# Kernel tuning notes

Measured on AMD Instinct MI355X. Metric: run time of the kernel, lower is better.

Reference implementation:

```python
import jax, jax.numpy as jnp
import numpy as np

N_NODES = 100000


def _gcn_conv(x, W, b, src, dst, n):
    # PyG GCNConv: add self-loops, sym-normalize by deg^{-1/2}, then X W + b
    h = x @ W  # [N, out]
    ones = jnp.ones(src.shape[0], dtype=x.dtype)
    deg = jax.ops.segment_sum(ones, dst, num_segments=n) + 1.0  # +1 for self loop
    dinv = jax.lax.rsqrt(deg)
    norm = dinv[src] * dinv[dst]  # [E]
    agg = jax.ops.segment_sum(h[src] * norm[:, None], dst, num_segments=n)
    agg = agg + h * (dinv * dinv)[:, None]  # self-loop contribution
    return agg + b


def setup_inputs() -> dict:
    key = jax.random.key(0)
    k1, k2, k3, k4 = jax.random.split(key, 4)
    n, e = N_NODES, 1600000
    in_d, hid_d, out_d = 128, 128, 64
    x = jax.random.normal(k1, (n, in_d), dtype=jnp.float32)
    edge_index = jax.random.randint(k2, (2, e), 0, n, dtype=jnp.int64)
    s1 = 1.0 / np.sqrt(in_d)
    s2 = 1.0 / np.sqrt(hid_d)
    W1 = jax.random.uniform(k3, (in_d, hid_d), jnp.float32, -s1, s1)
    W2 = jax.random.uniform(k4, (hid_d, out_d), jnp.float32, -s2, s2)
    b1 = jnp.zeros((hid_d,), jnp.float32)
    b2 = jnp.zeros((out_d,), jnp.float32)
    return {"x": x, "edge_index": edge_index, "W1": W1, "b1": b1, "W2": W2, "b2": b2}


def reference(x, edge_index, W1, b1, W2, b2):
    src, dst = edge_index[0], edge_index[1]
    n = x.shape[0]
    h = _gcn_conv(x, W1, b1, src, dst, n)
    h = jax.nn.relu(h)
    # dropout p=0.2 is identity at eval time
    out = _gcn_conv(h, W2, b2, src, dst, n)
    return out
```

## Files before the change

### kernel.cpp

```cpp
#include <hip/hip_runtime.h>


typedef unsigned int u32;
using bfrag = __attribute__((ext_vector_type(8))) short;
using f4    = __attribute__((ext_vector_type(4))) float;

__device__ inline u32 pack_bf16(float a, float b) {
    u32 ua = __float_as_uint(a);
    u32 ub = __float_as_uint(b);
    ua += 0x7fffu + ((ua >> 16) & 1u);
    ub += 0x7fffu + ((ub >> 16) & 1u);
    return (ua >> 16) | (ub & 0xffff0000u);
}
__device__ inline float bf_lo(u32 v) { return __uint_as_float(v << 16); }
__device__ inline float bf_hi(u32 v) { return __uint_as_float(v & 0xffff0000u); }

__device__ inline u32 pack_w(float w) {
    u32 b = __float_as_uint(w) + 0x800u;
    if (b < 0x3B800000u) b = 0x3B800000u;
    if (b > 0x3F800000u) b = 0x3F800000u;
    return (b - 0x3B800000u) >> 12;
}
__device__ inline float dec_w(u32 e) {
    return __uint_as_float(((e & 0x7fffu) << 12) + 0x3B800000u);
}

__device__ inline bfrag as_bfrag(uint4 v) {
    union { uint4 u; bfrag b; } x; x.u = v; return x.b;
}


__global__ __launch_bounds__(256) void count_bins_pw(const int* __restrict__ dst,
                                                     int* __restrict__ bc,
                                                     int E, int nbin, int nb3, int M,
                                                     const float* __restrict__ W1,
                                                     const float* __restrict__ W2,
                                                     u32* __restrict__ W1t,
                                                     u32* __restrict__ W2t) {
    __shared__ int hist[512];
    if (blockIdx.x >= (unsigned)nb3) {
        int idx = (blockIdx.x - nb3) * 256 + threadIdx.x;
        if (idx < 128 * 64) {
            int nr = idx >> 6, kd = idx & 63;
            W1t[idx] = pack_bf16(W1[(2 * kd) * 128 + nr], W1[(2 * kd + 1) * 128 + nr]);
        } else if (idx < 128 * 64 + 64 * 64) {
            int i = idx - 128 * 64;
            int nr = i >> 6, kd = i & 63;
            W2t[i] = pack_bf16(W2[(2 * kd) * 64 + nr], W2[(2 * kd + 1) * 64 + nr]);
        }
        return;
    }
    if (blockIdx.x == 0 && threadIdx.x == 0) bc[M] = E;
    for (int t = threadIdx.x; t < nbin; t += 256) hist[t] = 0;
    __syncthreads();
    const int base = blockIdx.x * 2048 + threadIdx.x;
#pragma unroll
    for (int k = 0; k < 8; ++k) {
        int e = base + k * 256;
        if (e < E) atomicAdd(&hist[dst[e] >> 8], 1);
    }
    __syncthreads();
    for (int t = threadIdx.x; t < nbin; t += 256)
        bc[(size_t)t * nb3 + blockIdx.x] = hist[t];
}

__global__ __launch_bounds__(1024) void scan_reduce_g(const int* __restrict__ a,
                                                      int* __restrict__ bsum, int M) {
    __shared__ int wsum[16];
    int i = blockIdx.x * 1024 + threadIdx.x;
    int v = (i < M) ? a[i] : 0;
#pragma unroll
    for (int off = 32; off > 0; off >>= 1) v += __shfl_down(v, off);
    const int lane = threadIdx.x & 63;
    const int wid  = threadIdx.x >> 6;
    if (lane == 0) wsum[wid] = v;
    __syncthreads();
    if (threadIdx.x < 16) {
        int s = wsum[threadIdx.x];
#pragma unroll
        for (int off = 8; off > 0; off >>= 1) s += __shfl_down(s, off);
        if (threadIdx.x == 0) bsum[blockIdx.x] = s;
    }
}

__global__ __launch_bounds__(1024) void scan_apply_g2(int* __restrict__ a,
                                                      const int* __restrict__ bsum,
                                                      int nb, int M) {
    __shared__ int wsum[16];
    __shared__ int base_s;
    const int lane = threadIdx.x & 63;
    const int wid  = threadIdx.x >> 6;

    int pv = 0;
    for (int t = threadIdx.x; t < (int)blockIdx.x; t += 1024) pv += bsum[t];
#pragma unroll
    for (int off = 32; off > 0; off >>= 1) pv += __shfl_down(pv, off);
    if (lane == 0) wsum[wid] = pv;
    __syncthreads();
    if (threadIdx.x == 0) {
        int s = 0;
#pragma unroll
        for (int w = 0; w < 16; ++w) s += wsum[w];
        base_s = s;
    }
    __syncthreads();
    const int boff = base_s;

    int i = blockIdx.x * 1024 + threadIdx.x;
    int v = (i < M) ? a[i] : 0;
    int x = v;
#pragma unroll
    for (int off = 1; off < 64; off <<= 1) {
        int t = __shfl_up(x, off);
        if (lane >= off) x += t;
    }
    if (lane == 63) wsum[wid] = x;
    __syncthreads();
    if (wid == 0 && lane < 16) {
        int w = wsum[lane];
#pragma unroll
        for (int off = 1; off < 16; off <<= 1) {
            int t = __shfl_up(w, off);
            if (lane >= off) w += t;
        }
        wsum[lane] = w;
    }
    __syncthreads();
    int wave_excl = (wid == 0) ? 0 : wsum[wid - 1];
    if (i < M) a[i] = boff + wave_excl + (x - v);
}

__global__ __launch_bounds__(1024) void scan_apply_cnt2(const int* __restrict__ cnt,
                                                        const int* __restrict__ bco,
                                                        int* __restrict__ row_ptr,
                                                        float* __restrict__ dinv,
                                                        int n, int nb3, int E) {
    __shared__ int wsum[16];
    const int lane = threadIdx.x & 63;
    const int wid  = threadIdx.x >> 6;
    const int boff = bco[(size_t)(4 * blockIdx.x) * nb3];
    int i = blockIdx.x * 1024 + threadIdx.x;
    int v = (i < n) ? cnt[i] : 0;
    int x = v;
#pragma unroll
    for (int off = 1; off < 64; off <<= 1) {
        int t = __shfl_up(x, off);
        if (lane >= off) x += t;
    }
    if (lane == 63) wsum[wid] = x;
    __syncthreads();
    if (wid == 0 && lane < 16) {
        int w = wsum[lane];
#pragma unroll
        for (int off = 1; off < 16; off <<= 1) {
            int t = __shfl_up(w, off);
            if (lane >= off) w += t;
        }
        wsum[lane] = w;
    }
    __syncthreads();
    int wave_excl = (wid == 0) ? 0 : wsum[wid - 1];
    if (i < n) {
        row_ptr[i] = boff + wave_excl + (x - v);
        dinv[i]    = rsqrtf((float)v + 1.0f);
    }
    if (blockIdx.x == 0 && threadIdx.x == 0) row_ptr[n] = E;
}

__global__ __launch_bounds__(256) void scatter_bins(const int* __restrict__ src,
                                                    const int* __restrict__ dst,
                                                    const int* __restrict__ offs,
                                                    u32* __restrict__ tmp,
                                                    int E, int nbin, int nb3) {
    __shared__ int cur[512];
    for (int t = threadIdx.x; t < nbin; t += 256)
        cur[t] = offs[(size_t)t * nb3 + blockIdx.x];
    __syncthreads();
    const int base = blockIdx.x * 2048 + threadIdx.x;
#pragma unroll
    for (int k = 0; k < 8; ++k) {
        int e = base + k * 256;
        if (e < E) {
            int d = dst[e];
            int pos = atomicAdd(&cur[d >> 8], 1);
            tmp[pos] = ((u32)(d & 255) << 17) | (u32)src[e];
        }
    }
}

__global__ __launch_bounds__(256) void bucket_csr(const u32* __restrict__ tmp,
                                                  const int* __restrict__ offs,
                                                  u32* __restrict__ tmp3,
                                                  int* __restrict__ cnt,
                                                  int n, int nb3) {
    __shared__ int hist[256];
    __shared__ int cur[256];
    __shared__ int wtot[4];
    const int b   = blockIdx.x;
    const int beg = offs[(size_t)b * nb3];
    const int end = offs[(size_t)(b + 1) * nb3];
    hist[threadIdx.x] = 0;
    __syncthreads();
    for (int i = beg + threadIdx.x; i < end; i += 256)
        atomicAdd(&hist[tmp[i] >> 17], 1);
    __syncthreads();
    const int lane = threadIdx.x & 63;
    const int wid  = threadIdx.x >> 6;
    int v = hist[threadIdx.x];
    int x = v;
#pragma unroll
    for (int off = 1; off < 64; off <<= 1) {
        int t = __shfl_up(x, off);
        if (lane >= off) x += t;
    }
    if (lane == 63) wtot[wid] = x;
    __syncthreads();
    int wbase = 0;
    for (int w = 0; w < wid; ++w) wbase += wtot[w];
    cur[threadIdx.x] = beg + wbase + x - v;
    int d = b * 256 + threadIdx.x;
    if (d < n) cnt[d] = v;
    __syncthreads();
    for (int i = beg + threadIdx.x; i < end; i += 256) {
        u32 r = tmp[i];
        int pos = atomicAdd(&cur[r >> 17], 1);
        tmp3[pos] = r & 0x1ffffu;
    }
}

__global__ __launch_bounds__(256) void build_ew(const u32* __restrict__ tmp3,
                                                const int* __restrict__ row_ptr,
                                                const float* __restrict__ dinv,
                                                u32* __restrict__ ew, int n) {
    int d = blockIdx.x * 256 + threadIdx.x;
    if (d >= n) return;
    float dd = dinv[d];
    int beg = row_ptr[d], end = row_ptr[d + 1];
    for (int i = beg; i < end; ++i) {
        u32 s = tmp3[i];
        ew[i] = (s << 15) | pack_w(dinv[s] * dd);
    }
}


template <int OUT, bool ABF>
__global__ __launch_bounds__(256) void gemm_mfma(const void* __restrict__ Ap,
                                                 const u32* __restrict__ Wt,
                                                 u32* __restrict__ C, int n) {
    constexpr int NT = OUT / 16;
    const int lane = threadIdx.x & 63;
    const int wv   = threadIdx.x >> 6;
    const int r15  = lane & 15;
    const int quad = lane >> 4;
    const int rowbase = blockIdx.x * 128 + wv * 32;

    bfrag af[2][4];
#pragma unroll
    for (int mi = 0; mi < 2; ++mi) {
        int row = rowbase + mi * 16 + r15;
        row = (row < n) ? row : (n - 1);
        if constexpr (ABF) {
            const u32* ar = (const u32*)Ap + (size_t)row * 64 + quad * 4;
#pragma unroll
            for (int ks = 0; ks < 4; ++ks)
                af[mi][ks] = as_bfrag(*(const uint4*)(ar + ks * 16));
        } else {
            const float* arf = (const float*)Ap + (size_t)row * 128 + quad * 8;
#pragma unroll
            for (int ks = 0; ks < 4; ++ks) {
                float4 v0 = *(const float4*)(arf + ks * 32);
                float4 v1 = *(const float4*)(arf + ks * 32 + 4);
                uint4 p;
                p.x = pack_bf16(v0.x, v0.y);
                p.y = pack_bf16(v0.z, v0.w);
                p.z = pack_bf16(v1.x, v1.y);
                p.w = pack_bf16(v1.z, v1.w);
                af[mi][ks] = as_bfrag(p);
            }
        }
    }

    f4 acc[2][NT];
#pragma unroll
    for (int mi = 0; mi < 2; ++mi)
#pragma unroll
        for (int nt = 0; nt < NT; ++nt) acc[mi][nt] = (f4)0.0f;

#pragma unroll
    for (int nt = 0; nt < NT; ++nt) {
        const u32* wr = Wt + (size_t)(nt * 16 + r15) * 64 + quad * 4;
#pragma unroll
        for (int ks = 0; ks < 4; ++ks) {
            bfrag bf = as_bfrag(*(const uint4*)(wr + ks * 16));
            acc[0][nt] = __builtin_amdgcn_mfma_f32_16x16x32_bf16(bf, af[0][ks], acc[0][nt], 0, 0, 0);
            acc[1][nt] = __builtin_amdgcn_mfma_f32_16x16x32_bf16(bf, af[1][ks], acc[1][nt], 0, 0, 0);
        }
    }

#pragma unroll
    for (int mi = 0; mi < 2; ++mi) {
        int row = rowbase + mi * 16 + r15;
        if (row < n) {
            u32* cp = C + (size_t)row * (OUT / 2);
#pragma unroll
            for (int nt = 0; nt < NT; ++nt) {
                uint2 p;
                p.x = pack_bf16(acc[mi][nt][0], acc[mi][nt][1]);
                p.y = pack_bf16(acc[mi][nt][2], acc[mi][nt][3]);
                *(uint2*)(cp + nt * 8 + quad * 2) = p;
            }
        }
    }
}


__global__ __launch_bounds__(256) void gather128(const u32* __restrict__ h,
                                                 const float* __restrict__ dinv,
                                                 const int* __restrict__ row_ptr,
                                                 const u32* __restrict__ ew,
                                                 const float* __restrict__ bias,
                                                 u32* __restrict__ outp, int n) {
    const int lane = threadIdx.x & 63;
    int node = blockIdx.x * 4 + (threadIdx.x >> 6);
    if (node >= n) return;
    node = __builtin_amdgcn_readfirstlane(node);

    const float dd  = dinv[node];
    const int   beg = __builtin_amdgcn_readfirstlane(row_ptr[node]);
    const int   end = __builtin_amdgcn_readfirstlane(row_ptr[node + 1]);

    u32 sv = h[(size_t)node * 64 + lane];
    float2 b = ((const float2*)bias)[lane];
    float acc0 = fmaf(bf_lo(sv) * dd, dd, b.x);
    float acc1 = fmaf(bf_hi(sv) * dd, dd, b.y);

    int j = beg;
    for (; j + 16 <= end; j += 16) {
        u32 ep[16];
#pragma unroll
        for (int k = 0; k < 16; ++k) ep[k] = ew[j + k];
        u32 v[16];
#pragma unroll
        for (int k = 0; k < 16; ++k)
            v[k] = h[((size_t)(ep[k] >> 15) << 6) + lane];
#pragma unroll
        for (int k = 0; k < 16; ++k) {
            float wf = dec_w(ep[k]);
            acc0 = fmaf(wf, bf_lo(v[k]), acc0);
            acc1 = fmaf(wf, bf_hi(v[k]), acc1);
        }
    }
    for (; j < end; j += 8) {
        const int cnt = end - j;
        u32 ep[8];
#pragma unroll
        for (int k = 0; k < 8; ++k) {
            int c = j + k;
            ep[k] = ew[(c < end) ? c : end - 1];
        }
        u32 v[8];
#pragma unroll
        for (int k = 0; k < 8; ++k)
            v[k] = h[((size_t)(ep[k] >> 15) << 6) + lane];
#pragma unroll
        for (int k = 0; k < 8; ++k) {
            float wf = (k < cnt) ? dec_w(ep[k]) : 0.0f;
            acc0 = fmaf(wf, bf_lo(v[k]), acc0);
            acc1 = fmaf(wf, bf_hi(v[k]), acc1);
        }
    }

    outp[(size_t)node * 64 + lane] = pack_bf16(fmaxf(acc0, 0.0f), fmaxf(acc1, 0.0f));
}

__global__ __launch_bounds__(256) void gather64(const u32* __restrict__ h,
                                                const float* __restrict__ dinv,
                                                const int* __restrict__ row_ptr,
                                                const u32* __restrict__ ew,
                                                const float* __restrict__ bias,
                                                float* __restrict__ outp, int n) {
    const int lane   = threadIdx.x & 63;
    const int lane32 = lane & 31;
    const int sub    = lane >> 5;
    int node = blockIdx.x * 4 + (threadIdx.x >> 6);
    if (node >= n) return;
    node = __builtin_amdgcn_readfirstlane(node);

    const int beg = __builtin_amdgcn_readfirstlane(row_ptr[node]);
    const int end = __builtin_amdgcn_readfirstlane(row_ptr[node + 1]);

    float acc0 = 0.0f, acc1 = 0.0f;
    if (sub == 0) {
        const float dd = dinv[node];
        u32 sv = h[(size_t)node * 32 + lane32];
        float2 b = ((const float2*)bias)[lane32];
        acc0 = fmaf(bf_lo(sv) * dd, dd, b.x);
        acc1 = fmaf(bf_hi(sv) * dd, dd, b.y);
    }

    int j = beg;
    for (; j + 16 <= end; j += 16) {
        u32 ep[16];
#pragma unroll
        for (int k = 0; k < 16; ++k) ep[k] = ew[j + k];
        u32 v[8]; float wl[8];
#pragma unroll
        for (int p = 0; p < 8; ++p) {
            u32 e0 = ep[2 * p], e1 = ep[2 * p + 1];
            u32 so = sub ? (e1 >> 15) : (e0 >> 15);
            wl[p]  = sub ? dec_w(e1) : dec_w(e0);
            v[p]   = h[((size_t)so << 5) + lane32];
        }
#pragma unroll
        for (int p = 0; p < 8; ++p) {
            acc0 = fmaf(wl[p], bf_lo(v[p]), acc0);
            acc1 = fmaf(wl[p], bf_hi(v[p]), acc1);
        }
    }
    for (; j < end; j += 8) {
        const int cnt = end - j;
        u32 ep[8];
#pragma unroll
        for (int k = 0; k < 8; ++k) {
            int c = j + k;
            ep[k] = ew[(c < end) ? c : end - 1];
        }
        u32 v[4]; float wl[4];
#pragma unroll
        for (int p = 0; p < 4; ++p) {
            u32 e0 = ep[2 * p], e1 = ep[2 * p + 1];
            float w0 = (2 * p     < cnt) ? dec_w(e0) : 0.0f;
            float w1 = (2 * p + 1 < cnt) ? dec_w(e1) : 0.0f;
            u32 so = sub ? (e1 >> 15) : (e0 >> 15);
            wl[p]  = sub ? w1 : w0;
            v[p]   = h[((size_t)so << 5) + lane32];
        }
#pragma unroll
        for (int p = 0; p < 4; ++p) {
            acc0 = fmaf(wl[p], bf_lo(v[p]), acc0);
            acc1 = fmaf(wl[p], bf_hi(v[p]), acc1);
        }
    }

    acc0 += __shfl_xor(acc0, 32);
    acc1 += __shfl_xor(acc1, 32);
    if (sub == 0)
        ((float2*)(outp + (size_t)node * 64))[lane32] = make_float2(acc0, acc1);
}

extern "C" void kernel_launch(void* const* d_in, const int* in_sizes, int n_in,
                              void* d_out, int out_size, void* d_ws, size_t ws_size,
                              hipStream_t stream) {
    const float* x  = (const float*)d_in[0];
    const int*   ei = (const int*)d_in[1];
    const float* W1 = (const float*)d_in[2];
    const float* b1 = (const float*)d_in[3];
    const float* W2 = (const float*)d_in[4];
    const float* b2 = (const float*)d_in[5];
    float*       out = (float*)d_out;

    const int n = in_sizes[0] / 128;
    const int E = in_sizes[1] / 2;
    const int* srcv = ei;
    const int* dstv = ei + E;

    const int NP = 102400;
    u32* wsd = (u32*)d_ws;
    float* dinv    = (float*)wsd;
    int*   row_ptr = (int*)(wsd + NP);
    u32*   ew      = wsd + 2 * (size_t)NP;
    u32*   h1u     = ew + E;
    u32*   agg1b   = h1u + (size_t)n * 64;
    u32*   W1t     = agg1b + (size_t)n * 64;
    u32*   W2t     = W1t + 8192;
    u32*   h2u     = h1u;

    int*   cnt  = (int*)h1u;
    int*   bco  = (int*)(h1u + 131072);
    u32*   tmp2 = h1u + 524288;
    u32*   tmp3 = tmp2 + (size_t)E;
    int*   bsum = (int*)(h1u + 4000000);

    const int NBIN = (n + 255) >> 8;
    const int NB3  = (E + 2047) / 2048;
    const int M    = NBIN * NB3;
    const int MB   = (M + 1023) / 1024;
    const int NB   = (n + 1023) / 1024;

    count_bins_pw<<<NB3 + 48, 256, 0, stream>>>(dstv, bco, E, NBIN, NB3, M,
                                                W1, W2, W1t, W2t);
    scan_reduce_g<<<MB, 1024, 0, stream>>>(bco, bsum, M);
    scan_apply_g2<<<MB, 1024, 0, stream>>>(bco, bsum, MB, M);
    scatter_bins<<<NB3, 256, 0, stream>>>(srcv, dstv, bco, tmp2, E, NBIN, NB3);
    bucket_csr<<<NBIN, 256, 0, stream>>>(tmp2, bco, tmp3, cnt, n, NB3);
    scan_apply_cnt2<<<NB, 1024, 0, stream>>>(cnt, bco, row_ptr, dinv, n, NB3, E);
    build_ew<<<(n + 255) / 256, 256, 0, stream>>>(tmp3, row_ptr, dinv, ew, n);

    const int gblocks = (n + 127) / 128;
    gemm_mfma<128, false><<<gblocks, 256, 0, stream>>>(x, W1t, h1u, n);
    gather128<<<(n + 3) / 4, 256, 0, stream>>>(h1u, dinv, row_ptr, ew, b1, agg1b, n);

    gemm_mfma<64, true><<<gblocks, 256, 0, stream>>>(agg1b, W2t, h2u, n);
    gather64<<<(n + 3) / 4, 256, 0, stream>>>(h2u, dinv, row_ptr, ew, b2, out, n);
}
```

Measured before the change: 302.0 us.

## Fuse CSR construction pipeline into one cooperative kernel with grid syncs

Replaces the seven separate CSR-building launches (bin count, two-stage scan, scatter, bucket sort, row pointer scan, edge weights) with a single cooperative kernel that separates the phases with grid.sync(). Its aim is to remove per-launch overhead and the idle gaps between small kernels. The original launch sequence stays as a fallback if the cooperative launch fails. The risk is that the grid of NB3 (782) blocks must be co-resident, and grid barriers add their own cost. The scan also assumes MB ≤ 512 and MB ≤ NB3, and the bucket phase assumes nbin ≤ NB3.

```diff
diff --git a/kernel.cpp b/kernel.cpp
--- a/kernel.cpp
+++ b/kernel.cpp
@@ -1,4 +1,5 @@
 #include <hip/hip_runtime.h>
+#include <hip/hip_cooperative_groups.h>
 
 
 typedef unsigned int u32;
@@ -27,6 +28,186 @@
 
 __device__ inline bfrag as_bfrag(uint4 v) {
     union { uint4 u; bfrag b; } x; x.u = v; return x.b;
+}
+
+__device__ inline void prep_w_chunk(int idx, const float* __restrict__ W1,
+                                    const float* __restrict__ W2,
+                                    u32* __restrict__ W1t, u32* __restrict__ W2t) {
+    if (idx < 128 * 64) {
+        int nr = idx >> 6, kd = idx & 63;
+        W1t[idx] = pack_bf16(W1[(2 * kd) * 128 + nr], W1[(2 * kd + 1) * 128 + nr]);
+    } else if (idx < 128 * 64 + 64 * 64) {
+        int i = idx - 128 * 64;
+        int nr = i >> 6, kd = i & 63;
+        W2t[i] = pack_bf16(W2[(2 * kd) * 64 + nr], W2[(2 * kd + 1) * 64 + nr]);
+    }
+}
+
+__global__ __launch_bounds__(256) void csr_coop(
+    const int* __restrict__ src, const int* __restrict__ dst,
+    int* __restrict__ bco, int* __restrict__ bsum,
+    u32* __restrict__ tmp2, u32* __restrict__ tmp3,
+    int* __restrict__ row_ptr, float* __restrict__ dinv, u32* __restrict__ ew,
+    const float* __restrict__ W1, const float* __restrict__ W2,
+    u32* __restrict__ W1t, u32* __restrict__ W2t,
+    int E, int n, int nbin, int nb3, int M, int MB)
+{
+    cooperative_groups::grid_group grid = cooperative_groups::this_grid();
+    const int b    = blockIdx.x;
+    const int t    = threadIdx.x;
+    const int lane = t & 63;
+    const int wid  = t >> 6;
+
+    __shared__ int   sh_cur[512];
+    __shared__ int   sh_h4[256];
+    __shared__ int   sh_c4[256];
+    __shared__ int   sh_w[16];
+    __shared__ int   sh_rp[257];
+    __shared__ float sh_di[256];
+    __shared__ int   sh_b;
+
+    {
+        for (int i = t; i < nbin; i += 256) sh_cur[i] = 0;
+        __syncthreads();
+        const int base = b * 2048 + t;
+#pragma unroll
+        for (int k = 0; k < 8; ++k) {
+            int e = base + k * 256;
+            if (e < E) atomicAdd(&sh_cur[dst[e] >> 8], 1);
+        }
+        __syncthreads();
+        for (int i = t; i < nbin; i += 256)
+            bco[(size_t)i * nb3 + b] = sh_cur[i];
+        if (b == 0 && t == 0) bco[M] = E;
+        if (b < 48) prep_w_chunk(b * 256 + t, W1, W2, W1t, W2t);
+    }
+    __threadfence();
+    grid.sync();
+
+    int v0 = 0, v1 = 0, v2 = 0, v3 = 0;
+    if (b < MB) {
+        const int i0 = b * 1024 + t * 4;
+        if (i0 + 3 < M) {
+            int4 q = *(const int4*)(bco + i0);
+            v0 = q.x; v1 = q.y; v2 = q.z; v3 = q.w;
+        } else {
+            if (i0     < M) v0 = bco[i0];
+            if (i0 + 1 < M) v1 = bco[i0 + 1];
+            if (i0 + 2 < M) v2 = bco[i0 + 2];
+            if (i0 + 3 < M) v3 = bco[i0 + 3];
+        }
+        int s = v0 + v1 + v2 + v3;
+#pragma unroll
+        for (int off = 32; off > 0; off >>= 1) s += __shfl_down(s, off);
+        if (lane == 0) sh_w[wid] = s;
+        __syncthreads();
+        if (t == 0) bsum[b] = sh_w[0] + sh_w[1] + sh_w[2] + sh_w[3];
+    }
+    __threadfence();
+    grid.sync();
+
+    if (b < MB) {
+        int pv = 0;
+        if (t < b)        pv += bsum[t];
+        if (t + 256 < b)  pv += bsum[t + 256];
+#pragma unroll
+        for (int off = 32; off > 0; off >>= 1) pv += __shfl_down(pv, off);
+        if (lane == 0) sh_w[wid] = pv;
+        __syncthreads();
+        if (t == 0) sh_b = sh_w[0] + sh_w[1] + sh_w[2] + sh_w[3];
+        __syncthreads();
+        const int blockoff = sh_b;
+        const int tv = v0 + v1 + v2 + v3;
+        int x = tv;
+#pragma unroll
+        for (int off = 1; off < 64; off <<= 1) {
+            int u = __shfl_up(x, off);
+            if (lane >= off) x += u;
+        }
+        if (lane == 63) sh_w[wid] = x;
+        __syncthreads();
+        int woff = 0;
+        for (int w2 = 0; w2 < wid; ++w2) woff += sh_w[w2];
+        int p = blockoff + woff + (x - tv);
+        const int i0 = b * 1024 + t * 4;
+        if (i0     < M) bco[i0]     = p;
+        if (i0 + 1 < M) bco[i0 + 1] = p + v0;
+        if (i0 + 2 < M) bco[i0 + 2] = p + v0 + v1;
+        if (i0 + 3 < M) bco[i0 + 3] = p + v0 + v1 + v2;
+    }
+    __threadfence();
+    grid.sync();
+
+    {
+        for (int i = t; i < nbin; i += 256)
+            sh_cur[i] = bco[(size_t)i * nb3 + b];
+        __syncthreads();
+        const int base = b * 2048 + t;
+#pragma unroll
+        for (int k = 0; k < 8; ++k) {
+            int e = base + k * 256;
+            if (e < E) {
+                int d = dst[e];
+                int pos = atomicAdd(&sh_cur[d >> 8], 1);
+                tmp2[pos] = ((u32)(d & 255) << 17) | (u32)src[e];
+            }
+        }
+    }
+    __threadfence();
+    grid.sync();
+
+    int binbeg = 0, binend = 0;
+    if (b < nbin) {
+        binbeg = bco[(size_t)b * nb3];
+        binend = bco[(size_t)(b + 1) * nb3];
+        sh_h4[t] = 0;
+        __syncthreads();
+        for (int i = binbeg + t; i < binend; i += 256)
+            atomicAdd(&sh_h4[tmp2[i] >> 17], 1);
+        __syncthreads();
+        int v = sh_h4[t];
+        int x = v;
+#pragma unroll
+        for (int off = 1; off < 64; off <<= 1) {
+            int u = __shfl_up(x, off);
+            if (lane >= off) x += u;
+        }
+        if (lane == 63) sh_w[wid] = x;
+        __syncthreads();
+        int woff = 0;
+        for (int w2 = 0; w2 < wid; ++w2) woff += sh_w[w2];
+        const int rp = binbeg + woff + (x - v);
+        sh_rp[t] = rp;
+        if (t == 255) sh_rp[256] = binend;
+        sh_c4[t] = rp;
+        const float di = rsqrtf((float)v + 1.0f);
+        sh_di[t] = di;
+        const int d = b * 256 + t;
+        if (d < n) { row_ptr[d] = rp; dinv[d] = di; }
+        if (b == 0 && t == 0) row_ptr[n] = E;
+        __syncthreads();
+        for (int i = binbeg + t; i < binend; i += 256) {
+            u32 r = tmp2[i];
+            int pos = atomicAdd(&sh_c4[r >> 17], 1);
+            tmp3[pos] = r & 0x1ffffu;
+        }
+    }
+    __threadfence();
+    grid.sync();
+
+    if (b < nbin) {
+        for (int i = binbeg + t; i < binend; i += 256) {
+            u32 s = tmp3[i];
+            int lo = 0, hi = 255;
+#pragma unroll
+            for (int st = 0; st < 8; ++st) {
+                int mid = (lo + hi + 1) >> 1;
+                if (sh_rp[mid] <= i) lo = mid; else hi = mid - 1;
+            }
+            float w = dinv[s] * sh_di[lo];
+            ew[i] = (s << 15) | pack_w(w);
+        }
+    }
 }
 
 
@@ -39,15 +220,7 @@
                                                      u32* __restrict__ W2t) {
     __shared__ int hist[512];
     if (blockIdx.x >= (unsigned)nb3) {
-        int idx = (blockIdx.x - nb3) * 256 + threadIdx.x;
-        if (idx < 128 * 64) {
-            int nr = idx >> 6, kd = idx & 63;
-            W1t[idx] = pack_bf16(W1[(2 * kd) * 128 + nr], W1[(2 * kd + 1) * 128 + nr]);
-        } else if (idx < 128 * 64 + 64 * 64) {
-            int i = idx - 128 * 64;
-            int nr = i >> 6, kd = i & 63;
-            W2t[i] = pack_bf16(W2[(2 * kd) * 64 + nr], W2[(2 * kd + 1) * 64 + nr]);
-        }
+        prep_w_chunk((blockIdx.x - nb3) * 256 + threadIdx.x, W1, W2, W1t, W2t);
         return;
     }
     if (blockIdx.x == 0 && threadIdx.x == 0) bc[M] = E;
@@ -90,7 +263,6 @@
     __shared__ int base_s;
     const int lane = threadIdx.x & 63;
     const int wid  = threadIdx.x >> 6;
-
     int pv = 0;
     for (int t = threadIdx.x; t < (int)blockIdx.x; t += 1024) pv += bsum[t];
 #pragma unroll
@@ -105,7 +277,6 @@
     }
     __syncthreads();
     const int boff = base_s;
-
     int i = blockIdx.x * 1024 + threadIdx.x;
     int v = (i < M) ? a[i] : 0;
     int x = v;
@@ -459,8 +630,8 @@
     const float* b2 = (const float*)d_in[5];
     float*       out = (float*)d_out;
 
-    const int n = in_sizes[0] / 128;
-    const int E = in_sizes[1] / 2;
+    int n = in_sizes[0] / 128;
+    int E = in_sizes[1] / 2;
     const int* srcv = ei;
     const int* dstv = ei + E;
 
@@ -481,20 +652,31 @@
     u32*   tmp3 = tmp2 + (size_t)E;
     int*   bsum = (int*)(h1u + 4000000);
 
-    const int NBIN = (n + 255) >> 8;
-    const int NB3  = (E + 2047) / 2048;
-    const int M    = NBIN * NB3;
-    const int MB   = (M + 1023) / 1024;
-    const int NB   = (n + 1023) / 1024;
-
-    count_bins_pw<<<NB3 + 48, 256, 0, stream>>>(dstv, bco, E, NBIN, NB3, M,
-                                                W1, W2, W1t, W2t);
-    scan_reduce_g<<<MB, 1024, 0, stream>>>(bco, bsum, M);
-    scan_apply_g2<<<MB, 1024, 0, stream>>>(bco, bsum, MB, M);
-    scatter_bins<<<NB3, 256, 0, stream>>>(srcv, dstv, bco, tmp2, E, NBIN, NB3);
-    bucket_csr<<<NBIN, 256, 0, stream>>>(tmp2, bco, tmp3, cnt, n, NB3);
-    scan_apply_cnt2<<<NB, 1024, 0, stream>>>(cnt, bco, row_ptr, dinv, n, NB3, E);
-    build_ew<<<(n + 255) / 256, 256, 0, stream>>>(tmp3, row_ptr, dinv, ew, n);
+    int NBIN = (n + 255) >> 8;
+    int NB3  = (E + 2047) / 2048;
+    int M    = NBIN * NB3;
+    int MB   = (M + 1023) / 1024;
+    const int NB = (n + 1023) / 1024;
+
+    void* cargs[] = {
+        (void*)&srcv, (void*)&dstv, (void*)&bco, (void*)&bsum,
+        (void*)&tmp2, (void*)&tmp3, (void*)&row_ptr, (void*)&dinv, (void*)&ew,
+        (void*)&W1, (void*)&W2, (void*)&W1t, (void*)&W2t,
+        (void*)&E, (void*)&n, (void*)&NBIN, (void*)&NB3, (void*)&M, (void*)&MB
+    };
+    hipError_t cerr = hipLaunchCooperativeKernel((const void*)csr_coop,
+                                                 dim3(NB3), dim3(256),
+                                                 cargs, 0, stream);
+    if (cerr != hipSuccess) {
+        count_bins_pw<<<NB3 + 48, 256, 0, stream>>>(dstv, bco, E, NBIN, NB3, M,
+                                                    W1, W2, W1t, W2t);
+        scan_reduce_g<<<MB, 1024, 0, stream>>>(bco, bsum, M);
+        scan_apply_g2<<<MB, 1024, 0, stream>>>(bco, bsum, MB, M);
+        scatter_bins<<<NB3, 256, 0, stream>>>(srcv, dstv, bco, tmp2, E, NBIN, NB3);
+        bucket_csr<<<NBIN, 256, 0, stream>>>(tmp2, bco, tmp3, cnt, n, NB3);
+        scan_apply_cnt2<<<NB, 1024, 0, stream>>>(cnt, bco, row_ptr, dinv, n, NB3, E);
+        build_ew<<<(n + 255) / 256, 256, 0, stream>>>(tmp3, row_ptr, dinv, ew, n);
+    }
 
     const int gblocks = (n + 127) / 128;
     gemm_mfma<128, false><<<gblocks, 256, 0, stream>>>(x, W1t, h1u, n);
```

After: 1.092 ms. +261.5%, slower.

## Fold row_ptr/dinv scan into bucket_csr and parallelize edge-weight build per edge

Applied to the files above, without the earlier changes.

The per-bucket exclusive scan in bucket_csr already gives global row offsets, so row_ptr and dinv are now written there directly and the separate scan_apply_cnt2 kernel is removed. build_ew is rewritten so each block covers one 256-node bucket, caches row_ptr and dinv in shared memory, and assigns edges to threads with coalesced strides. Each thread finds its destination row by binary search. This removes one launch and replaces the per-node serial edge loop, which had poor coalescing and load imbalance, at the cost of eight shared-memory search steps per edge.

```diff
diff --git a/kernel.cpp b/kernel.cpp
--- a/kernel.cpp
+++ b/kernel.cpp
@@ -27,6 +27,19 @@
 
 __device__ inline bfrag as_bfrag(uint4 v) {
     union { uint4 u; bfrag b; } x; x.u = v; return x.b;
+}
+
+__device__ inline void prep_w_chunk(int idx, const float* __restrict__ W1,
+                                    const float* __restrict__ W2,
+                                    u32* __restrict__ W1t, u32* __restrict__ W2t) {
+    if (idx < 128 * 64) {
+        int nr = idx >> 6, kd = idx & 63;
+        W1t[idx] = pack_bf16(W1[(2 * kd) * 128 + nr], W1[(2 * kd + 1) * 128 + nr]);
+    } else if (idx < 128 * 64 + 64 * 64) {
+        int i = idx - 128 * 64;
+        int nr = i >> 6, kd = i & 63;
+        W2t[i] = pack_bf16(W2[(2 * kd) * 64 + nr], W2[(2 * kd + 1) * 64 + nr]);
+    }
 }
 
 
@@ -39,15 +52,7 @@
                                                      u32* __restrict__ W2t) {
     __shared__ int hist[512];
     if (blockIdx.x >= (unsigned)nb3) {
-        int idx = (blockIdx.x - nb3) * 256 + threadIdx.x;
-        if (idx < 128 * 64) {
-            int nr = idx >> 6, kd = idx & 63;
-            W1t[idx] = pack_bf16(W1[(2 * kd) * 128 + nr], W1[(2 * kd + 1) * 128 + nr]);
-        } else if (idx < 128 * 64 + 64 * 64) {
-            int i = idx - 128 * 64;
-            int nr = i >> 6, kd = i & 63;
-            W2t[i] = pack_bf16(W2[(2 * kd) * 64 + nr], W2[(2 * kd + 1) * 64 + nr]);
-        }
+        prep_w_chunk((blockIdx.x - nb3) * 256 + threadIdx.x, W1, W2, W1t, W2t);
         return;
     }
     if (blockIdx.x == 0 && threadIdx.x == 0) bc[M] = E;
@@ -90,7 +95,6 @@
     __shared__ int base_s;
     const int lane = threadIdx.x & 63;
     const int wid  = threadIdx.x >> 6;
-
     int pv = 0;
     for (int t = threadIdx.x; t < (int)blockIdx.x; t += 1024) pv += bsum[t];
 #pragma unroll
@@ -105,7 +109,6 @@
     }
     __syncthreads();
     const int boff = base_s;
-
     int i = blockIdx.x * 1024 + threadIdx.x;
     int v = (i < M) ? a[i] : 0;
     int x = v;
@@ -128,43 +131,6 @@
     __syncthreads();
     int wave_excl = (wid == 0) ? 0 : wsum[wid - 1];
     if (i < M) a[i] = boff + wave_excl + (x - v);
-}
-
-__global__ __launch_bounds__(1024) void scan_apply_cnt2(const int* __restrict__ cnt,
-                                                        const int* __restrict__ bco,
-                                                        int* __restrict__ row_ptr,
-                                                        float* __restrict__ dinv,
-                                                        int n, int nb3, int E) {
-    __shared__ int wsum[16];
-    const int lane = threadIdx.x & 63;
-    const int wid  = threadIdx.x >> 6;
-    const int boff = bco[(size_t)(4 * blockIdx.x) * nb3];
-    int i = blockIdx.x * 1024 + threadIdx.x;
-    int v = (i < n) ? cnt[i] : 0;
-    int x = v;
-#pragma unroll
-    for (int off = 1; off < 64; off <<= 1) {
-        int t = __shfl_up(x, off);
-        if (lane >= off) x += t;
-    }
-    if (lane == 63) wsum[wid] = x;
-    __syncthreads();
-    if (wid == 0 && lane < 16) {
-        int w = wsum[lane];
-#pragma unroll
-        for (int off = 1; off < 16; off <<= 1) {
-            int t = __shfl_up(w, off);
-            if (lane >= off) w += t;
-        }
-        wsum[lane] = w;
-    }
-    __syncthreads();
-    int wave_excl = (wid == 0) ? 0 : wsum[wid - 1];
-    if (i < n) {
-        row_ptr[i] = boff + wave_excl + (x - v);
-        dinv[i]    = rsqrtf((float)v + 1.0f);
-    }
-    if (blockIdx.x == 0 && threadIdx.x == 0) row_ptr[n] = E;
 }
 
 __global__ __launch_bounds__(256) void scatter_bins(const int* __restrict__ src,
@@ -188,11 +154,12 @@
     }
 }
 
-__global__ __launch_bounds__(256) void bucket_csr(const u32* __restrict__ tmp,
-                                                  const int* __restrict__ offs,
-                                                  u32* __restrict__ tmp3,
-                                                  int* __restrict__ cnt,
-                                                  int n, int nb3) {
+__global__ __launch_bounds__(256) void bucket_csr2(const u32* __restrict__ tmp,
+                                                   const int* __restrict__ offs,
+                                                   u32* __restrict__ tmp3,
+                                                   int* __restrict__ row_ptr,
+                                                   float* __restrict__ dinv,
+                                                   int n, int nb3, int E) {
     __shared__ int hist[256];
     __shared__ int cur[256];
     __shared__ int wtot[4];
@@ -217,9 +184,14 @@
     __syncthreads();
     int wbase = 0;
     for (int w = 0; w < wid; ++w) wbase += wtot[w];
-    cur[threadIdx.x] = beg + wbase + x - v;
-    int d = b * 256 + threadIdx.x;
-    if (d < n) cnt[d] = v;
+    const int rp = beg + wbase + x - v;
+    cur[threadIdx.x] = rp;
+    const int d = b * 256 + threadIdx.x;
+    if (d < n) {
+        row_ptr[d] = rp;
+        dinv[d]    = rsqrtf((float)v + 1.0f);
+    }
+    if (b == 0 && threadIdx.x == 0) row_ptr[n] = E;
     __syncthreads();
     for (int i = beg + threadIdx.x; i < end; i += 256) {
         u32 r = tmp[i];
@@ -228,17 +200,34 @@
     }
 }
 
-__global__ __launch_bounds__(256) void build_ew(const u32* __restrict__ tmp3,
-                                                const int* __restrict__ row_ptr,
-                                                const float* __restrict__ dinv,
-                                                u32* __restrict__ ew, int n) {
-    int d = blockIdx.x * 256 + threadIdx.x;
-    if (d >= n) return;
-    float dd = dinv[d];
-    int beg = row_ptr[d], end = row_ptr[d + 1];
-    for (int i = beg; i < end; ++i) {
+__global__ __launch_bounds__(256) void build_ew2(const u32* __restrict__ tmp3,
+                                                 const int* __restrict__ row_ptr,
+                                                 const float* __restrict__ dinv,
+                                                 u32* __restrict__ ew, int n) {
+    __shared__ int   sh_rp[257];
+    __shared__ float sh_di[256];
+    const int b = blockIdx.x;
+    const int t = threadIdx.x;
+    const int base = b * 256;
+    const int idx  = base + t;
+    sh_rp[t] = row_ptr[(idx <= n) ? idx : n];
+    if (t == 0) {
+        int last = base + 256;
+        sh_rp[256] = row_ptr[(last <= n) ? last : n];
+    }
+    sh_di[t] = (idx < n) ? dinv[idx] : 0.0f;
+    __syncthreads();
+    const int beg = sh_rp[0];
+    const int end = sh_rp[256];
+    for (int i = beg + t; i < end; i += 256) {
         u32 s = tmp3[i];
-        ew[i] = (s << 15) | pack_w(dinv[s] * dd);
+        int lo = 0, hi = 255;
+#pragma unroll
+        for (int st = 0; st < 8; ++st) {
+            int mid = (lo + hi + 1) >> 1;
+            if (sh_rp[mid] <= i) lo = mid; else hi = mid - 1;
+        }
+        ew[i] = (s << 15) | pack_w(dinv[s] * sh_di[lo]);
     }
 }
 
@@ -475,7 +464,6 @@
     u32*   W2t     = W1t + 8192;
     u32*   h2u     = h1u;
 
-    int*   cnt  = (int*)h1u;
     int*   bco  = (int*)(h1u + 131072);
     u32*   tmp2 = h1u + 524288;
     u32*   tmp3 = tmp2 + (size_t)E;
@@ -485,16 +473,14 @@
     const int NB3  = (E + 2047) / 2048;
     const int M    = NBIN * NB3;
     const int MB   = (M + 1023) / 1024;
-    const int NB   = (n + 1023) / 1024;
 
     count_bins_pw<<<NB3 + 48, 256, 0, stream>>>(dstv, bco, E, NBIN, NB3, M,
                                                 W1, W2, W1t, W2t);
     scan_reduce_g<<<MB, 1024, 0, stream>>>(bco, bsum, M);
     scan_apply_g2<<<MB, 1024, 0, stream>>>(bco, bsum, MB, M);
     scatter_bins<<<NB3, 256, 0, stream>>>(srcv, dstv, bco, tmp2, E, NBIN, NB3);
-    bucket_csr<<<NBIN, 256, 0, stream>>>(tmp2, bco, tmp3, cnt, n, NB3);
-    scan_apply_cnt2<<<NB, 1024, 0, stream>>>(cnt, bco, row_ptr, dinv, n, NB3, E);
-    build_ew<<<(n + 255) / 256, 256, 0, stream>>>(tmp3, row_ptr, dinv, ew, n);
+    bucket_csr2<<<NBIN, 256, 0, stream>>>(tmp2, bco, tmp3, row_ptr, dinv, n, NB3, E);
+    build_ew2<<<NBIN, 256, 0, stream>>>(tmp3, row_ptr, dinv, ew, n);
 
     const int gblocks = (n + 127) / 128;
     gemm_mfma<128, false><<<gblocks, 256, 0, stream>>>(x, W1t, h1u, n);
```

New measurement: 294.1 us. 1.03x faster.
